# Kernel optimization log

Hardware: AMD Instinct MI355X
Metric: run time of the kernel (lower is better)

The kernel has to match this reference:

```python
import jax, jax.numpy as jnp
import numpy as np

B, N, K_OUT, NBASIS, NGLOBALS, H = 16, 2048, 128, 4, 2, 256
DIN = 1 + NBASIS + N + NGLOBALS  # norm + basis projections + all-pairs dots + globals
NEG_SLOPE = 0.01  # torch LeakyReLU default


def setup_inputs() -> dict:
    key = jax.random.key(0)
    ks = jax.random.split(key, 6)
    x = jax.random.uniform(ks[0], (B, N, 3), jnp.float32)      # positions -> dots >= 0
    u = jax.random.normal(ks[1], (B, NGLOBALS), jnp.float32)
    basis = jax.random.normal(ks[2], (B, NBASIS, 3), jnp.float32)
    def init_w(k, fan_in, fan_out):
        return jax.random.normal(k, (fan_in, fan_out), jnp.float32) / np.float32(np.sqrt(fan_in))
    W1 = init_w(ks[3], DIN, H); b1 = jnp.zeros((H,), jnp.float32)
    W2 = init_w(ks[4], H, H);   b2 = jnp.zeros((H,), jnp.float32)
    W3 = init_w(ks[5], H, K_OUT); b3 = jnp.zeros((K_OUT,), jnp.float32)
    return {"x": x, "u": u, "basis": basis,
            "W1": W1, "b1": b1, "W2": W2, "b2": b2, "W3": W3, "b3": b3}


def reference(x, u, basis, W1, b1, W2, b2, W3, b3):
    # per-vector norms: [B, N, 1]
    norms = jnp.linalg.norm(x, axis=-1, keepdims=True)
    # projections onto basis vectors: [B, N, NBASIS]
    proj = jnp.einsum('bid,bnd->bin', x, basis)
    # all-pairs sqrt of dot products: [B, N, N]
    dots = jnp.sqrt(jnp.einsum('bid,bjd->bij', x, x))
    # concat order matches original: globals first, then [norm, proj, dots]
    u_rep = jnp.broadcast_to(u[:, None, :], (B, N, NGLOBALS))
    scalars = jnp.concatenate([u_rep, norms, proj, dots], axis=-1)  # [B, N, DIN]
    # MLP (Linear -> LeakyReLU -> Linear -> LeakyReLU -> Linear)
    h = jax.nn.leaky_relu(scalars @ W1 + b1, NEG_SLOPE)
    h = jax.nn.leaky_relu(h @ W2 + b2, NEG_SLOPE)
    fk = h @ W3 + b3  # [B, N, K_OUT]
    # outer product with x followed by mean over input vecs, fused into one einsum
    # (avoids materializing the [B, N, K_OUT, 3] tensor)
    return jnp.einsum('bio,bid->bod', fk, x) / np.float32(N)  # [B, K_OUT, 3]
```

## Files before the change

kernel.cpp:

```cpp
#include <hip/hip_runtime.h>

typedef unsigned short u16;
typedef unsigned int   u32;

typedef __attribute__((ext_vector_type(8))) short short8;
typedef __attribute__((ext_vector_type(4))) float floatx4;
typedef __attribute__((ext_vector_type(2))) float v2f;

__device__ __forceinline__ u16 f2bf(float f) {
    u32 u = __float_as_uint(f);
    u = u + 0x7fffu + ((u >> 16) & 1u);
    return (u16)(u >> 16);
}

__device__ __forceinline__ u32 pack2bf(float s0, float s1) {
    u32 a = __float_as_uint(s0) + 0x8000u;
    u32 b = __float_as_uint(s1) + 0x8000u;
    return __builtin_amdgcn_perm(b, a, 0x07060302u);
}

__device__ __forceinline__ floatx4 mfma16(short8 a, short8 b, floatx4 c) {
    return __builtin_amdgcn_mfma_f32_16x16x32_bf16(a, b, c, 0, 0, 0);
}

__global__ void k_prep(const float* __restrict__ W1, const float* __restrict__ W2,
                       const float* __restrict__ W3, u16* __restrict__ W1frag,
                       u16* __restrict__ W2frag, u16* __restrict__ W3frag,
                       float* __restrict__ out) {
    int idx = blockIdx.x * 256 + threadIdx.x;
    if (idx < 6144) out[idx] = 0.f;
    if (idx < 524288) {
        int row = idx >> 8, c = idx & 255;
        float v = W1[1792 + idx];
        int kt = row >> 5, rr = row & 31;
        int lq = rr >> 3, ji = rr & 7;
        int w = c >> 5, cc = c & 31;
        int j = cc >> 4, lr = cc & 15;
        W1frag[kt * 8192 + (w * 64 + lq * 16 + lr) * 16 + j * 8 + ji] = f2bf(v);
    } else if (idx < 589824) {
        int i = idx - 524288;
        int row = i >> 8, c = i & 255;
        float v = W2[i];
        int kt = row >> 5, rr = row & 31;
        int lq = rr >> 3, ji = rr & 7;
        int w = c >> 5, cc = c & 31;
        int j = cc >> 4, lr = cc & 15;
        W2frag[kt * 8192 + (w * 64 + lq * 16 + lr) * 16 + j * 8 + ji] = f2bf(v);
    } else if (idx < 622592) {
        int i = idx - 589824;
        int row = i >> 7, c = i & 127;
        float v = W3[i];
        int kt = row >> 5, rr = row & 31;
        int lq = rr >> 3, ji = rr & 7;
        int w = c >> 4, lr = c & 15;
        W3frag[kt * 4096 + (w * 64 + lq * 16 + lr) * 8 + ji] = f2bf(v);
    }
}

__global__ __launch_bounds__(512, 4) void k_fused(
    const float* __restrict__ x, const float* __restrict__ u,
    const float* __restrict__ basis, const float* __restrict__ W1,
    const float* __restrict__ b1, const float* __restrict__ b2,
    const float* __restrict__ b3, const u16* __restrict__ W1frag,
    const u16* __restrict__ W2frag, const u16* __restrict__ W3frag,
    float* __restrict__ out) {
    __shared__ __align__(16) char smem[76288];
    float* xls = (float*)smem;
    char* Asb = smem + 24576;
    u16 (*h1s)[264] = (u16(*)[264])smem;
    float (*xsm)[4] = (float(*)[4])(smem + 33792);
    float (*redm)[4] = (float(*)[4])(smem + 34816);
    float (*rowsml)[6] = (float(*)[6])(smem + 40960);
    float (*colsml)[8] = (float(*)[8])(smem + 42496);
    u16 (*h2s)[264] = (u16(*)[264])(smem + 42496);

    const int t = threadIdx.x;
    const int b = blockIdx.y;
    const int i0 = blockIdx.x * 64;
    const int lane = t & 63, w = t >> 6;
    const int lr = lane & 15, lq = lane >> 4;

    {
        const float4* src = (const float4*)(x + b * 6144);
#pragma unroll
        for (int kk = 0; kk < 3; ++kk) {
            int q = t + kk * 512;
            float4 v = src[q];
            float vv[4] = {v.x, v.y, v.z, v.w};
            int e = q * 4;
#pragma unroll
            for (int cc = 0; cc < 4; ++cc) {
                int ee = e + cc;
                xls[(ee % 3) * 2048 + ee / 3] = vv[cc];
            }
        }
    }
    if (t < 256) {
        int c = t;
        float u0 = u[b * 2 + 0], u1 = u[b * 2 + 1];
        colsml[c][0] = b1[c] + u0 * W1[c] + u1 * W1[256 + c];
        colsml[c][1] = W1[512 + c];
        colsml[c][2] = W1[768 + c];
        colsml[c][3] = W1[1024 + c];
        colsml[c][4] = W1[1280 + c];
        colsml[c][5] = W1[1536 + c];
        colsml[c][6] = b2[c];
        if (c < 128) colsml[c][7] = b3[c];
    }
    __syncthreads();
    if (t < 64) {
        float xx = xls[i0 + t], xy = xls[2048 + i0 + t], xz = xls[4096 + i0 + t];
        rowsml[t][0] = sqrtf(xx * xx + xy * xy + xz * xz);
#pragma unroll
        for (int p = 0; p < 4; ++p) {
            const float* bp = basis + (b * 4 + p) * 3;
            rowsml[t][1 + p] = xx * bp[0] + xy * bp[1] + xz * bp[2];
        }
    }
    const float ax = xls[i0 + lane];
    const float ay = xls[2048 + i0 + lane];
    const float az = xls[4096 + i0 + lane];
    const u16* wf = W1frag + t * 16;
    const float4* X4 = (const float4*)xls;

    char* aswp = Asb + lane * 128 + ((w ^ (lane & 7)) << 4);
    int ro[4];
    {
        int sl = (lq ^ (lr & 7));
#pragma unroll
        for (int i = 0; i < 4; ++i)
            ro[i] = (i * 16 + lr) * 128 + (sl << 4);
    }

    auto gen_store = [&](int s, int buf) {
        int q = s * 16 + w * 2;
        v2f dA, dB, dC, dD;
        {
            float4 a0 = X4[q], a1 = X4[q + 1];
            v2f t0 = {a0.x, a0.y}, t1 = {a0.z, a0.w};
            v2f t2 = {a1.x, a1.y}, t3 = {a1.z, a1.w};
            dA = t0 * ax; dB = t1 * ax; dC = t2 * ax; dD = t3 * ax;
        }
        {
            float4 a0 = X4[512 + q], a1 = X4[513 + q];
            v2f t0 = {a0.x, a0.y}, t1 = {a0.z, a0.w};
            v2f t2 = {a1.x, a1.y}, t3 = {a1.z, a1.w};
            dA += t0 * ay; dB += t1 * ay; dC += t2 * ay; dD += t3 * ay;
        }
        {
            float4 a0 = X4[1024 + q], a1 = X4[1025 + q];
            v2f t0 = {a0.x, a0.y}, t1 = {a0.z, a0.w};
            v2f t2 = {a1.x, a1.y}, t3 = {a1.z, a1.w};
            dA += t0 * az; dB += t1 * az; dC += t2 * az; dD += t3 * az;
        }
        float s0 = __builtin_amdgcn_sqrtf(dA.x);
        float s1 = __builtin_amdgcn_sqrtf(dA.y);
        float s2 = __builtin_amdgcn_sqrtf(dB.x);
        float s3 = __builtin_amdgcn_sqrtf(dB.y);
        float s4 = __builtin_amdgcn_sqrtf(dC.x);
        float s5 = __builtin_amdgcn_sqrtf(dC.y);
        float s6 = __builtin_amdgcn_sqrtf(dD.x);
        float s7 = __builtin_amdgcn_sqrtf(dD.y);
        uint4 dv;
        dv.x = pack2bf(s0, s1); dv.y = pack2bf(s2, s3);
        dv.z = pack2bf(s4, s5); dv.w = pack2bf(s6, s7);
        *(uint4*)(aswp + buf * 8192) = dv;
    };

    floatx4 acc[4][2];
    const floatx4 zero = {0.f, 0.f, 0.f, 0.f};
#pragma unroll
    for (int i = 0; i < 4; ++i)
#pragma unroll
        for (int j = 0; j < 2; ++j) acc[i][j] = zero;

    gen_store(0, 0);
    __syncthreads();

    {
        short8 a0[4], a1[4], bfr[4];
#pragma unroll 2
        for (int s = 0; s < 32; ++s) {
            const int buf = s & 1;
            const u16* wb = wf + (2 * s) * 8192;
            bfr[0] = *(const short8*)(wb);
            bfr[1] = *(const short8*)(wb + 8);
            bfr[2] = *(const short8*)(wb + 8192);
            bfr[3] = *(const short8*)(wb + 8192 + 8);
#pragma unroll
            for (int i = 0; i < 4; ++i)
                a0[i] = *(const short8*)(Asb + buf * 8192 + ro[i]);
#pragma unroll
            for (int i = 0; i < 4; ++i)
                a1[i] = *(const short8*)(Asb + buf * 8192 + (ro[i] ^ 64));
            if (s < 31) gen_store(s + 1, buf ^ 1);
#pragma unroll
            for (int i = 0; i < 4; ++i)
#pragma unroll
                for (int j = 0; j < 2; ++j)
                    acc[i][j] = mfma16(a0[i], bfr[j], acc[i][j]);
#pragma unroll
            for (int i = 0; i < 4; ++i)
#pragma unroll
                for (int j = 0; j < 2; ++j)
                    acc[i][j] = mfma16(a1[i], bfr[2 + j], acc[i][j]);
            __syncthreads();
        }
    }

    if (t < 64) { xsm[t][0] = ax; xsm[t][1] = ay; xsm[t][2] = az; }
    const int c0 = w * 32 + lr, c1 = c0 + 16;
    const int c3 = w * 16 + lr;
    float cb0, cb1, cb3;
    {
        float c0v[7], c1v[7];
#pragma unroll
        for (int q = 0; q < 7; ++q) { c0v[q] = colsml[c0][q]; c1v[q] = colsml[c1][q]; }
        cb0 = c0v[6]; cb1 = c1v[6];
        cb3 = colsml[c3][7];
#pragma unroll
        for (int i = 0; i < 4; ++i) {
#pragma unroll
            for (int r = 0; r < 4; ++r) {
                int row = i * 16 + lq * 4 + r;
                float nrm = rowsml[row][0];
                float p0 = rowsml[row][1], p1 = rowsml[row][2];
                float p2 = rowsml[row][3], p3 = rowsml[row][4];
                float v0 = acc[i][0][r] + c0v[0] + nrm * c0v[1] +
                           p0 * c0v[2] + p1 * c0v[3] + p2 * c0v[4] + p3 * c0v[5];
                v0 = v0 > 0.f ? v0 : 0.01f * v0;
                h1s[row][c0] = f2bf(v0);
                float v1 = acc[i][1][r] + c1v[0] + nrm * c1v[1] +
                           p0 * c1v[2] + p1 * c1v[3] + p2 * c1v[4] + p3 * c1v[5];
                v1 = v1 > 0.f ? v1 : 0.01f * v1;
                h1s[row][c1] = f2bf(v1);
            }
        }
    }
    __syncthreads();

#pragma unroll
    for (int i = 0; i < 4; ++i)
#pragma unroll
        for (int j = 0; j < 2; ++j) acc[i][j] = zero;
    {
        const u16* w2s = W2frag + t * 16;
#pragma unroll 2
        for (int kt = 0; kt < 8; ++kt) {
            short8 af[4], bfr[2];
#pragma unroll
            for (int i = 0; i < 4; ++i)
                af[i] = *(const short8*)&h1s[i * 16 + lr][kt * 32 + lq * 8];
#pragma unroll
            for (int j = 0; j < 2; ++j)
                bfr[j] = *(const short8*)(w2s + kt * 8192 + j * 8);
#pragma unroll
            for (int i = 0; i < 4; ++i)
#pragma unroll
                for (int j = 0; j < 2; ++j)
                    acc[i][j] = mfma16(af[i], bfr[j], acc[i][j]);
        }
#pragma unroll
        for (int i = 0; i < 4; ++i)
#pragma unroll
            for (int r = 0; r < 4; ++r) {
                int row = i * 16 + lq * 4 + r;
                float v0 = acc[i][0][r] + cb0;
                v0 = v0 > 0.f ? v0 : 0.01f * v0;
                h2s[row][c0] = f2bf(v0);
                float v1 = acc[i][1][r] + cb1;
                v1 = v1 > 0.f ? v1 : 0.01f * v1;
                h2s[row][c1] = f2bf(v1);
            }
    }
    __syncthreads();

    {
        floatx4 acc2[4];
#pragma unroll
        for (int i = 0; i < 4; ++i) acc2[i] = zero;
        const u16* w3s = W3frag + t * 8;
#pragma unroll 2
        for (int kt = 0; kt < 8; ++kt) {
            short8 af[4];
#pragma unroll
            for (int i = 0; i < 4; ++i)
                af[i] = *(const short8*)&h2s[i * 16 + lr][kt * 32 + lq * 8];
            short8 bfr = *(const short8*)(w3s + kt * 4096);
#pragma unroll
            for (int i = 0; i < 4; ++i) acc2[i] = mfma16(af[i], bfr, acc2[i]);
        }
        float s0 = 0.f, s1 = 0.f, s2 = 0.f;
#pragma unroll
        for (int i = 0; i < 4; ++i)
#pragma unroll
            for (int r = 0; r < 4; ++r) {
                int row = i * 16 + lq * 4 + r;
                float fk = acc2[i][r] + cb3;
                s0 += fk * xsm[row][0];
                s1 += fk * xsm[row][1];
                s2 += fk * xsm[row][2];
            }
        s0 += __shfl_xor(s0, 16); s0 += __shfl_xor(s0, 32);
        s1 += __shfl_xor(s1, 16); s1 += __shfl_xor(s1, 32);
        s2 += __shfl_xor(s2, 16); s2 += __shfl_xor(s2, 32);
        if (lq == 0) {
            redm[c3][0] = s0; redm[c3][1] = s1; redm[c3][2] = s2;
        }
    }
    __syncthreads();
    if (t < 128) {
#pragma unroll
        for (int d = 0; d < 3; ++d)
            atomicAdd(&out[(b * 128 + t) * 3 + d], redm[t][d] * (1.0f / 2048.0f));
    }
}

extern "C" void kernel_launch(void* const* d_in, const int* in_sizes, int n_in,
                              void* d_out, int out_size, void* d_ws, size_t ws_size,
                              hipStream_t stream) {
    const float* x     = (const float*)d_in[0];
    const float* u     = (const float*)d_in[1];
    const float* basis = (const float*)d_in[2];
    const float* W1    = (const float*)d_in[3];
    const float* b1    = (const float*)d_in[4];
    const float* W2    = (const float*)d_in[5];
    const float* b2    = (const float*)d_in[6];
    const float* W3    = (const float*)d_in[7];
    const float* b3    = (const float*)d_in[8];
    float* out = (float*)d_out;

    char* ws = (char*)d_ws;
    u16*  W1frag = (u16*)ws;
    u16*  W2frag = (u16*)(ws + 1048576);
    u16*  W3frag = (u16*)(ws + 1179648);

    k_prep<<<2432, 256, 0, stream>>>(W1, W2, W3, W1frag, W2frag, W3frag, out);
    k_fused<<<dim3(32, 16), 512, 0, stream>>>(x, u, basis, W1, b1, b2, b3,
                                              W1frag, W2frag, W3frag, out);
}
```

Measured before the change: 122.1 us.

## Transpose x to SoA in prep kernel and retile layer-1 MFMA as 2x4 warp grid

The prep kernel now also writes x in structure-of-arrays order to the workspace, so the fused kernel reads dot-product operands directly from global/L2 instead of first staging the whole per-batch x into LDS. This removes the initial shuffle and one barrier. The layer-1 GEMM warp tiling changes from each warp covering all 64 rows by 32 columns to a 2x4 grid (32 rows by 64 columns). That halves the A-fragment LDS reads per warp but doubles the W1 fragment global loads. The gen_store path now issues global loads per step, which may add latency inside the main loop.

Result: slower. 131.7 us (+7.9%).

```diff
diff --git a/kernel.cpp b/kernel.cpp
--- a/kernel.cpp
+++ b/kernel.cpp
@@ -23,22 +23,28 @@
     return __builtin_amdgcn_mfma_f32_16x16x32_bf16(a, b, c, 0, 0, 0);
 }
 
-__global__ void k_prep(const float* __restrict__ W1, const float* __restrict__ W2,
-                       const float* __restrict__ W3, u16* __restrict__ W1frag,
+__global__ void k_prep(const float* __restrict__ x, const float* __restrict__ W1,
+                       const float* __restrict__ W2, const float* __restrict__ W3,
+                       float* __restrict__ xsoa, u16* __restrict__ W1frag,
                        u16* __restrict__ W2frag, u16* __restrict__ W3frag,
                        float* __restrict__ out) {
     int idx = blockIdx.x * 256 + threadIdx.x;
     if (idx < 6144) out[idx] = 0.f;
-    if (idx < 524288) {
-        int row = idx >> 8, c = idx & 255;
-        float v = W1[1792 + idx];
+    if (idx < 98304) {
+        int b = idx / 6144, r = idx - b * 6144;
+        int comp = r >> 11, n = r & 2047;
+        xsoa[idx] = x[(b * 2048 + n) * 3 + comp];
+    } else if (idx < 622592) {
+        int i = idx - 98304;
+        int row = i >> 8, c = i & 255;
+        float v = W1[1792 + i];
         int kt = row >> 5, rr = row & 31;
         int lq = rr >> 3, ji = rr & 7;
         int w = c >> 5, cc = c & 31;
         int j = cc >> 4, lr = cc & 15;
         W1frag[kt * 8192 + (w * 64 + lq * 16 + lr) * 16 + j * 8 + ji] = f2bf(v);
-    } else if (idx < 589824) {
-        int i = idx - 524288;
+    } else if (idx < 688128) {
+        int i = idx - 622592;
         int row = i >> 8, c = i & 255;
         float v = W2[i];
         int kt = row >> 5, rr = row & 31;
@@ -46,8 +52,8 @@
         int w = c >> 5, cc = c & 31;
         int j = cc >> 4, lr = cc & 15;
         W2frag[kt * 8192 + (w * 64 + lq * 16 + lr) * 16 + j * 8 + ji] = f2bf(v);
-    } else if (idx < 622592) {
-        int i = idx - 589824;
+    } else if (idx < 720896) {
+        int i = idx - 688128;
         int row = i >> 7, c = i & 127;
         float v = W3[i];
         int kt = row >> 5, rr = row & 31;
@@ -58,14 +64,13 @@
 }
 
 __global__ __launch_bounds__(512, 4) void k_fused(
-    const float* __restrict__ x, const float* __restrict__ u,
+    const float* __restrict__ xsoa, const float* __restrict__ u,
     const float* __restrict__ basis, const float* __restrict__ W1,
     const float* __restrict__ b1, const float* __restrict__ b2,
     const float* __restrict__ b3, const u16* __restrict__ W1frag,
     const u16* __restrict__ W2frag, const u16* __restrict__ W3frag,
     float* __restrict__ out) {
     __shared__ __align__(16) char smem[76288];
-    float* xls = (float*)smem;
     char* Asb = smem + 24576;
     u16 (*h1s)[264] = (u16(*)[264])smem;
     float (*xsm)[4] = (float(*)[4])(smem + 33792);
@@ -79,22 +84,13 @@
     const int i0 = blockIdx.x * 64;
     const int lane = t & 63, w = t >> 6;
     const int lr = lane & 15, lq = lane >> 4;
-
-    {
-        const float4* src = (const float4*)(x + b * 6144);
-#pragma unroll
-        for (int kk = 0; kk < 3; ++kk) {
-            int q = t + kk * 512;
-            float4 v = src[q];
-            float vv[4] = {v.x, v.y, v.z, v.w};
-            int e = q * 4;
-#pragma unroll
-            for (int cc = 0; cc < 4; ++cc) {
-                int ee = e + cc;
-                xls[(ee % 3) * 2048 + ee / 3] = vv[cc];
-            }
-        }
-    }
+    const int wm = w >> 2, wn = w & 3;
+
+    const float* Xg = xsoa + b * 6144;
+    const float ax = Xg[i0 + lane];
+    const float ay = Xg[2048 + i0 + lane];
+    const float az = Xg[4096 + i0 + lane];
+
     if (t < 256) {
         int c = t;
         float u0 = u[b * 2 + 0], u1 = u[b * 2 + 1];
@@ -107,48 +103,42 @@
         colsml[c][6] = b2[c];
         if (c < 128) colsml[c][7] = b3[c];
     }
-    __syncthreads();
     if (t < 64) {
-        float xx = xls[i0 + t], xy = xls[2048 + i0 + t], xz = xls[4096 + i0 + t];
-        rowsml[t][0] = sqrtf(xx * xx + xy * xy + xz * xz);
+        rowsml[t][0] = sqrtf(ax * ax + ay * ay + az * az);
 #pragma unroll
         for (int p = 0; p < 4; ++p) {
             const float* bp = basis + (b * 4 + p) * 3;
-            rowsml[t][1 + p] = xx * bp[0] + xy * bp[1] + xz * bp[2];
-        }
-    }
-    const float ax = xls[i0 + lane];
-    const float ay = xls[2048 + i0 + lane];
-    const float az = xls[4096 + i0 + lane];
-    const u16* wf = W1frag + t * 16;
-    const float4* X4 = (const float4*)xls;
+            rowsml[t][1 + p] = ax * bp[0] + ay * bp[1] + az * bp[2];
+        }
+    }
 
     char* aswp = Asb + lane * 128 + ((w ^ (lane & 7)) << 4);
-    int ro[4];
+    int roA[2];
     {
         int sl = (lq ^ (lr & 7));
 #pragma unroll
-        for (int i = 0; i < 4; ++i)
-            ro[i] = (i * 16 + lr) * 128 + (sl << 4);
+        for (int i = 0; i < 2; ++i)
+            roA[i] = (wm * 32 + i * 16 + lr) * 128 + (sl << 4);
     }
 
     auto gen_store = [&](int s, int buf) {
-        int q = s * 16 + w * 2;
+        int c0u = __builtin_amdgcn_readfirstlane(s * 64 + w * 8);
+        const float* Xc = Xg + c0u;
         v2f dA, dB, dC, dD;
         {
-            float4 a0 = X4[q], a1 = X4[q + 1];
+            float4 a0 = *(const float4*)(Xc), a1 = *(const float4*)(Xc + 4);
             v2f t0 = {a0.x, a0.y}, t1 = {a0.z, a0.w};
             v2f t2 = {a1.x, a1.y}, t3 = {a1.z, a1.w};
             dA = t0 * ax; dB = t1 * ax; dC = t2 * ax; dD = t3 * ax;
         }
         {
-            float4 a0 = X4[512 + q], a1 = X4[513 + q];
+            float4 a0 = *(const float4*)(Xc + 2048), a1 = *(const float4*)(Xc + 2052);
             v2f t0 = {a0.x, a0.y}, t1 = {a0.z, a0.w};
             v2f t2 = {a1.x, a1.y}, t3 = {a1.z, a1.w};
             dA += t0 * ay; dB += t1 * ay; dC += t2 * ay; dD += t3 * ay;
         }
         {
-            float4 a0 = X4[1024 + q], a1 = X4[1025 + q];
+            float4 a0 = *(const float4*)(Xc + 4096), a1 = *(const float4*)(Xc + 4100);
             v2f t0 = {a0.x, a0.y}, t1 = {a0.z, a0.w};
             v2f t2 = {a1.x, a1.y}, t3 = {a1.z, a1.w};
             dA += t0 * az; dB += t1 * az; dC += t2 * az; dD += t3 * az;
@@ -167,43 +157,47 @@
         *(uint4*)(aswp + buf * 8192) = dv;
     };
 
-    floatx4 acc[4][2];
+    floatx4 acc[2][4];
     const floatx4 zero = {0.f, 0.f, 0.f, 0.f};
 #pragma unroll
-    for (int i = 0; i < 4; ++i)
-#pragma unroll
-        for (int j = 0; j < 2; ++j) acc[i][j] = zero;
+    for (int i = 0; i < 2; ++i)
+#pragma unroll
+        for (int j = 0; j < 4; ++j) acc[i][j] = zero;
 
     gen_store(0, 0);
     __syncthreads();
 
     {
-        short8 a0[4], a1[4], bfr[4];
+        const u16* wfB = W1frag + (wn * 2 * 64 + lane) * 16;
+        short8 a0[2], a1[2], bfr[8];
 #pragma unroll 2
         for (int s = 0; s < 32; ++s) {
             const int buf = s & 1;
-            const u16* wb = wf + (2 * s) * 8192;
+            const u16* wb = wfB + (2 * s) * 8192;
             bfr[0] = *(const short8*)(wb);
             bfr[1] = *(const short8*)(wb + 8);
-            bfr[2] = *(const short8*)(wb + 8192);
-            bfr[3] = *(const short8*)(wb + 8192 + 8);
-#pragma unroll
-            for (int i = 0; i < 4; ++i)
-                a0[i] = *(const short8*)(Asb + buf * 8192 + ro[i]);
-#pragma unroll
-            for (int i = 0; i < 4; ++i)
-                a1[i] = *(const short8*)(Asb + buf * 8192 + (ro[i] ^ 64));
+            bfr[2] = *(const short8*)(wb + 1024);
+            bfr[3] = *(const short8*)(wb + 1024 + 8);
+            bfr[4] = *(const short8*)(wb + 8192);
+            bfr[5] = *(const short8*)(wb + 8192 + 8);
+            bfr[6] = *(const short8*)(wb + 8192 + 1024);
+            bfr[7] = *(const short8*)(wb + 8192 + 1024 + 8);
+#pragma unroll
+            for (int i = 0; i < 2; ++i) {
+                a0[i] = *(const short8*)(Asb + buf * 8192 + roA[i]);
+                a1[i] = *(const short8*)(Asb + buf * 8192 + (roA[i] ^ 64));
+            }
             if (s < 31) gen_store(s + 1, buf ^ 1);
 #pragma unroll
-            for (int i = 0; i < 4; ++i)
-#pragma unroll
-                for (int j = 0; j < 2; ++j)
+            for (int i = 0; i < 2; ++i)
+#pragma unroll
+                for (int j = 0; j < 4; ++j)
                     acc[i][j] = mfma16(a0[i], bfr[j], acc[i][j]);
 #pragma unroll
-            for (int i = 0; i < 4; ++i)
-#pragma unroll
-                for (int j = 0; j < 2; ++j)
-                    acc[i][j] = mfma16(a1[i], bfr[2 + j], acc[i][j]);
+            for (int i = 0; i < 2; ++i)
+#pragma unroll
+                for (int j = 0; j < 4; ++j)
+                    acc[i][j] = mfma16(a1[i], bfr[4 + j], acc[i][j]);
             __syncthreads();
         }
     }
@@ -213,37 +207,42 @@
     const int c3 = w * 16 + lr;
     float cb0, cb1, cb3;
     {
-        float c0v[7], c1v[7];
-#pragma unroll
-        for (int q = 0; q < 7; ++q) { c0v[q] = colsml[c0][q]; c1v[q] = colsml[c1][q]; }
-        cb0 = c0v[6]; cb1 = c1v[6];
+        float cv[4][6];
+#pragma unroll
+        for (int j = 0; j < 4; ++j) {
+            int c = wn * 64 + j * 16 + lr;
+#pragma unroll
+            for (int q = 0; q < 6; ++q) cv[j][q] = colsml[c][q];
+        }
+        cb0 = colsml[c0][6]; cb1 = colsml[c1][6];
         cb3 = colsml[c3][7];
 #pragma unroll
-        for (int i = 0; i < 4; ++i) {
+        for (int i = 0; i < 2; ++i) {
 #pragma unroll
             for (int r = 0; r < 4; ++r) {
-                int row = i * 16 + lq * 4 + r;
+                int row = wm * 32 + i * 16 + lq * 4 + r;
                 float nrm = rowsml[row][0];
                 float p0 = rowsml[row][1], p1 = rowsml[row][2];
                 float p2 = rowsml[row][3], p3 = rowsml[row][4];
-                float v0 = acc[i][0][r] + c0v[0] + nrm * c0v[1] +
-                           p0 * c0v[2] + p1 * c0v[3] + p2 * c0v[4] + p3 * c0v[5];
-                v0 = v0 > 0.f ? v0 : 0.01f * v0;
-                h1s[row][c0] = f2bf(v0);
-                float v1 = acc[i][1][r] + c1v[0] + nrm * c1v[1] +
-                           p0 * c1v[2] + p1 * c1v[3] + p2 * c1v[4] + p3 * c1v[5];
-                v1 = v1 > 0.f ? v1 : 0.01f * v1;
-                h1s[row][c1] = f2bf(v1);
+#pragma unroll
+                for (int j = 0; j < 4; ++j) {
+                    float v = acc[i][j][r] + cv[j][0] + nrm * cv[j][1] +
+                              p0 * cv[j][2] + p1 * cv[j][3] + p2 * cv[j][4] +
+                              p3 * cv[j][5];
+                    v = v > 0.f ? v : 0.01f * v;
+                    h1s[row][wn * 64 + j * 16 + lr] = f2bf(v);
+                }
             }
         }
     }
     __syncthreads();
 
-#pragma unroll
-    for (int i = 0; i < 4; ++i)
-#pragma unroll
-        for (int j = 0; j < 2; ++j) acc[i][j] = zero;
-    {
+    {
+        floatx4 accT[4][2];
+#pragma unroll
+        for (int i = 0; i < 4; ++i)
+#pragma unroll
+            for (int j = 0; j < 2; ++j) accT[i][j] = zero;
         const u16* w2s = W2frag + t * 16;
 #pragma unroll 2
         for (int kt = 0; kt < 8; ++kt) {
@@ -258,17 +257,17 @@
             for (int i = 0; i < 4; ++i)
 #pragma unroll
                 for (int j = 0; j < 2; ++j)
-                    acc[i][j] = mfma16(af[i], bfr[j], acc[i][j]);
+                    accT[i][j] = mfma16(af[i], bfr[j], accT[i][j]);
         }
 #pragma unroll
         for (int i = 0; i < 4; ++i)
 #pragma unroll
             for (int r = 0; r < 4; ++r) {
                 int row = i * 16 + lq * 4 + r;
-                float v0 = acc[i][0][r] + cb0;
+                float v0 = accT[i][0][r] + cb0;
                 v0 = v0 > 0.f ? v0 : 0.01f * v0;
                 h2s[row][c0] = f2bf(v0);
-                float v1 = acc[i][1][r] + cb1;
+                float v1 = accT[i][1][r] + cb1;
                 v1 = v1 > 0.f ? v1 : 0.01f * v1;
                 h2s[row][c1] = f2bf(v1);
             }
@@ -334,8 +333,10 @@
     u16*  W1frag = (u16*)ws;
     u16*  W2frag = (u16*)(ws + 1048576);
     u16*  W3frag = (u16*)(ws + 1179648);
-
-    k_prep<<<2432, 256, 0, stream>>>(W1, W2, W3, W1frag, W2frag, W3frag, out);
-    k_fused<<<dim3(32, 16), 512, 0, stream>>>(x, u, basis, W1, b1, b2, b3,
+    float* xsoa  = (float*)(ws + 1245184);
+
+    k_prep<<<2816, 256, 0, stream>>>(x, W1, W2, W3, xsoa, W1frag, W2frag,
+                                     W3frag, out);
+    k_fused<<<dim3(32, 16), 512, 0, stream>>>(xsoa, u, basis, W1, b1, b2, b3,
                                               W1frag, W2frag, W3frag, out);
 }
```

## Pre-transpose x to SoA in prep kernel and read it from global in GEMM loop

Applied to the files above, without the earlier changes.

The prep kernel now also writes x into a structure-of-arrays layout in workspace. The fused kernel no longer stages x into shared memory at startup; it reads its row values and the per-step column vectors directly from global/L2 using a wave-uniform base. This removes the startup LDS transposition and one barrier, and frees LDS reads in the inner loop. The A-fragment loads are also split into two halves interleaved with the MFMAs to lower register pressure. The cost is global-memory latency inside the generation step of the main loop, plus a larger prep grid.

Result: no change. 123.4 us (+1.1%).

```diff
diff --git a/kernel.cpp b/kernel.cpp
--- a/kernel.cpp
+++ b/kernel.cpp
@@ -23,22 +23,28 @@
     return __builtin_amdgcn_mfma_f32_16x16x32_bf16(a, b, c, 0, 0, 0);
 }
 
-__global__ void k_prep(const float* __restrict__ W1, const float* __restrict__ W2,
-                       const float* __restrict__ W3, u16* __restrict__ W1frag,
+__global__ void k_prep(const float* __restrict__ x, const float* __restrict__ W1,
+                       const float* __restrict__ W2, const float* __restrict__ W3,
+                       float* __restrict__ xsoa, u16* __restrict__ W1frag,
                        u16* __restrict__ W2frag, u16* __restrict__ W3frag,
                        float* __restrict__ out) {
     int idx = blockIdx.x * 256 + threadIdx.x;
     if (idx < 6144) out[idx] = 0.f;
-    if (idx < 524288) {
-        int row = idx >> 8, c = idx & 255;
-        float v = W1[1792 + idx];
+    if (idx < 98304) {
+        int b = idx / 6144, r = idx - b * 6144;
+        int comp = r >> 11, n = r & 2047;
+        xsoa[idx] = x[(b * 2048 + n) * 3 + comp];
+    } else if (idx < 622592) {
+        int i = idx - 98304;
+        int row = i >> 8, c = i & 255;
+        float v = W1[1792 + i];
         int kt = row >> 5, rr = row & 31;
         int lq = rr >> 3, ji = rr & 7;
         int w = c >> 5, cc = c & 31;
         int j = cc >> 4, lr = cc & 15;
         W1frag[kt * 8192 + (w * 64 + lq * 16 + lr) * 16 + j * 8 + ji] = f2bf(v);
-    } else if (idx < 589824) {
-        int i = idx - 524288;
+    } else if (idx < 688128) {
+        int i = idx - 622592;
         int row = i >> 8, c = i & 255;
         float v = W2[i];
         int kt = row >> 5, rr = row & 31;
@@ -46,8 +52,8 @@
         int w = c >> 5, cc = c & 31;
         int j = cc >> 4, lr = cc & 15;
         W2frag[kt * 8192 + (w * 64 + lq * 16 + lr) * 16 + j * 8 + ji] = f2bf(v);
-    } else if (idx < 622592) {
-        int i = idx - 589824;
+    } else if (idx < 720896) {
+        int i = idx - 688128;
         int row = i >> 7, c = i & 127;
         float v = W3[i];
         int kt = row >> 5, rr = row & 31;
@@ -58,14 +64,13 @@
 }
 
 __global__ __launch_bounds__(512, 4) void k_fused(
-    const float* __restrict__ x, const float* __restrict__ u,
+    const float* __restrict__ xsoa, const float* __restrict__ u,
     const float* __restrict__ basis, const float* __restrict__ W1,
     const float* __restrict__ b1, const float* __restrict__ b2,
     const float* __restrict__ b3, const u16* __restrict__ W1frag,
     const u16* __restrict__ W2frag, const u16* __restrict__ W3frag,
     float* __restrict__ out) {
     __shared__ __align__(16) char smem[76288];
-    float* xls = (float*)smem;
     char* Asb = smem + 24576;
     u16 (*h1s)[264] = (u16(*)[264])smem;
     float (*xsm)[4] = (float(*)[4])(smem + 33792);
@@ -80,21 +85,11 @@
     const int lane = t & 63, w = t >> 6;
     const int lr = lane & 15, lq = lane >> 4;
 
-    {
-        const float4* src = (const float4*)(x + b * 6144);
-#pragma unroll
-        for (int kk = 0; kk < 3; ++kk) {
-            int q = t + kk * 512;
-            float4 v = src[q];
-            float vv[4] = {v.x, v.y, v.z, v.w};
-            int e = q * 4;
-#pragma unroll
-            for (int cc = 0; cc < 4; ++cc) {
-                int ee = e + cc;
-                xls[(ee % 3) * 2048 + ee / 3] = vv[cc];
-            }
-        }
-    }
+    const float* Xg = xsoa + b * 6144;
+    const float ax = Xg[i0 + lane];
+    const float ay = Xg[2048 + i0 + lane];
+    const float az = Xg[4096 + i0 + lane];
+
     if (t < 256) {
         int c = t;
         float u0 = u[b * 2 + 0], u1 = u[b * 2 + 1];
@@ -107,21 +102,14 @@
         colsml[c][6] = b2[c];
         if (c < 128) colsml[c][7] = b3[c];
     }
-    __syncthreads();
     if (t < 64) {
-        float xx = xls[i0 + t], xy = xls[2048 + i0 + t], xz = xls[4096 + i0 + t];
-        rowsml[t][0] = sqrtf(xx * xx + xy * xy + xz * xz);
+        rowsml[t][0] = sqrtf(ax * ax + ay * ay + az * az);
 #pragma unroll
         for (int p = 0; p < 4; ++p) {
             const float* bp = basis + (b * 4 + p) * 3;
-            rowsml[t][1 + p] = xx * bp[0] + xy * bp[1] + xz * bp[2];
-        }
-    }
-    const float ax = xls[i0 + lane];
-    const float ay = xls[2048 + i0 + lane];
-    const float az = xls[4096 + i0 + lane];
-    const u16* wf = W1frag + t * 16;
-    const float4* X4 = (const float4*)xls;
+            rowsml[t][1 + p] = ax * bp[0] + ay * bp[1] + az * bp[2];
+        }
+    }
 
     char* aswp = Asb + lane * 128 + ((w ^ (lane & 7)) << 4);
     int ro[4];
@@ -133,22 +121,23 @@
     }
 
     auto gen_store = [&](int s, int buf) {
-        int q = s * 16 + w * 2;
+        int c0u = __builtin_amdgcn_readfirstlane(s * 64 + w * 8);
+        const float* Xc = Xg + c0u;
         v2f dA, dB, dC, dD;
         {
-            float4 a0 = X4[q], a1 = X4[q + 1];
+            float4 a0 = *(const float4*)(Xc), a1 = *(const float4*)(Xc + 4);
             v2f t0 = {a0.x, a0.y}, t1 = {a0.z, a0.w};
             v2f t2 = {a1.x, a1.y}, t3 = {a1.z, a1.w};
             dA = t0 * ax; dB = t1 * ax; dC = t2 * ax; dD = t3 * ax;
         }
         {
-            float4 a0 = X4[512 + q], a1 = X4[513 + q];
+            float4 a0 = *(const float4*)(Xc + 2048), a1 = *(const float4*)(Xc + 2052);
             v2f t0 = {a0.x, a0.y}, t1 = {a0.z, a0.w};
             v2f t2 = {a1.x, a1.y}, t3 = {a1.z, a1.w};
             dA += t0 * ay; dB += t1 * ay; dC += t2 * ay; dD += t3 * ay;
         }
         {
-            float4 a0 = X4[1024 + q], a1 = X4[1025 + q];
+            float4 a0 = *(const float4*)(Xc + 4096), a1 = *(const float4*)(Xc + 4100);
             v2f t0 = {a0.x, a0.y}, t1 = {a0.z, a0.w};
             v2f t2 = {a1.x, a1.y}, t3 = {a1.z, a1.w};
             dA += t0 * az; dB += t1 * az; dC += t2 * az; dD += t3 * az;
@@ -178,7 +167,8 @@
     __syncthreads();
 
     {
-        short8 a0[4], a1[4], bfr[4];
+        const u16* wf = W1frag + t * 16;
+        short8 a[4], bfr[4];
 #pragma unroll 2
         for (int s = 0; s < 32; ++s) {
             const int buf = s & 1;
@@ -189,21 +179,21 @@
             bfr[3] = *(const short8*)(wb + 8192 + 8);
 #pragma unroll
             for (int i = 0; i < 4; ++i)
-                a0[i] = *(const short8*)(Asb + buf * 8192 + ro[i]);
-#pragma unroll
-            for (int i = 0; i < 4; ++i)
-                a1[i] = *(const short8*)(Asb + buf * 8192 + (ro[i] ^ 64));
+                a[i] = *(const short8*)(Asb + buf * 8192 + ro[i]);
             if (s < 31) gen_store(s + 1, buf ^ 1);
 #pragma unroll
             for (int i = 0; i < 4; ++i)
 #pragma unroll
                 for (int j = 0; j < 2; ++j)
-                    acc[i][j] = mfma16(a0[i], bfr[j], acc[i][j]);
+                    acc[i][j] = mfma16(a[i], bfr[j], acc[i][j]);
+#pragma unroll
+            for (int i = 0; i < 4; ++i)
+                a[i] = *(const short8*)(Asb + buf * 8192 + (ro[i] ^ 64));
 #pragma unroll
             for (int i = 0; i < 4; ++i)
 #pragma unroll
                 for (int j = 0; j < 2; ++j)
-                    acc[i][j] = mfma16(a1[i], bfr[2 + j], acc[i][j]);
+                    acc[i][j] = mfma16(a[i], bfr[2 + j], acc[i][j]);
             __syncthreads();
         }
     }
@@ -334,8 +324,10 @@
     u16*  W1frag = (u16*)ws;
     u16*  W2frag = (u16*)(ws + 1048576);
     u16*  W3frag = (u16*)(ws + 1179648);
-
-    k_prep<<<2432, 256, 0, stream>>>(W1, W2, W3, W1frag, W2frag, W3frag, out);
-    k_fused<<<dim3(32, 16), 512, 0, stream>>>(x, u, basis, W1, b1, b2, b3,
+    float* xsoa  = (float*)(ws + 1245184);
+
+    k_prep<<<2816, 256, 0, stream>>>(x, W1, W2, W3, xsoa, W1frag, W2frag,
+                                     W3frag, out);
+    k_fused<<<dim3(32, 16), 512, 0, stream>>>(xsoa, u, basis, W1, b1, b2, b3,
                                               W1frag, W2frag, W3frag, out);
 }
```
